# Optimization experiments

Hardware: AMD Instinct MI355X
Metric: run time of the kernel (lower is better)

The kernel has to match this reference:

```python
import jax, jax.numpy as jnp
import numpy as np

N_HEADS = 8
PROJ_DIM = 32


def _phi(x):
    # elu(x) + 1 feature map (always > 0)
    return jax.nn.elu(x) + 1.0


def _causal_linear(pq, pk, v):
    # Faithful to torch _linear_kernelized_attention masked branch:
    #   dpq_l = pq_l - pq_{l-1} (with pq_{-1}=0)
    #   result_l = cumsum_{m<=l} (dpq_m . v_m) * pk_m
    # The torch code materializes (N,H,L,D,D); here the identical math is
    # computed via a per-position scalar c_m = dpq_m . v_m, O(L*D) memory.
    dpq = pq - jnp.concatenate([jnp.zeros_like(pq[..., :1, :]), pq[..., :-1, :]], axis=-2)
    c = jnp.einsum('nhld,nhld->nhl', dpq, v)[..., None]  # (N,H,L,1)
    return jnp.cumsum(c * pk, axis=-2)  # (N,H,L,D)


def _bidir_linear(pq, pk, v):
    # Non-masked linear path: (pk^T v) first, then pq @ (.)
    right = jnp.einsum('nhld,nhle->nhde', pk, v)
    return jnp.einsum('nhqd,nhde->nhqe', pq, right)


def _attention(Y, X, Wq, Wk, Wv, mask):
    N, Lq, Dm = Y.shape
    Lk = X.shape[1]
    H, Pd = N_HEADS, PROJ_DIM
    # torch Linear: x @ W^T
    q = (Y @ Wq.T).reshape(N, Lq, H, Pd).transpose(0, 2, 1, 3)  # (N,H,Lq,Pd)
    k = (X @ Wk.T).reshape(N, Lk, H, Pd).transpose(0, 2, 1, 3)
    v = (X @ Wv.T).reshape(N, Lk, H, Pd).transpose(0, 2, 1, 3)
    pq, pk = _phi(q), _phi(k)
    fn = _causal_linear if mask else _bidir_linear
    num = fn(pq, pk, v)
    den = fn(pq, pk, jnp.ones_like(v))  # v_scale = ones expanded to D
    A = num / den
    return A.transpose(0, 2, 1, 3).reshape(N, Lq, H * Pd)


def setup_inputs() -> dict:
    key = jax.random.key(0)
    kY, kX, kq, kk, kv = jax.random.split(key, 5)
    N, L, dim = 2, 8192, N_HEADS * PROJ_DIM
    scale_in = 0.05            # keep phi(q),phi(k) ~ 1 so denominator stays positive
    scale_w = 1.0 / np.sqrt(dim)
    Y = scale_in * jax.random.normal(kY, (N, L, dim), dtype=jnp.float32)
    X = scale_in * jax.random.normal(kX, (N, L, dim), dtype=jnp.float32)
    Wq = scale_w * jax.random.normal(kq, (dim, dim), dtype=jnp.float32)
    Wk = scale_w * jax.random.normal(kk, (dim, dim), dtype=jnp.float32)
    Wv = scale_w * jax.random.normal(kv, (dim, dim), dtype=jnp.float32)
    return {"Y": Y, "X": X, "Wq": Wq, "Wk": Wk, "Wv": Wv, "mask": 1}


def reference(Y, X, Wq, Wk, Wv, mask):
    return _attention(Y, X, Wq, Wk, Wv, mask)
```

## Files before the change

kernel.cpp:

```cpp
#include <hip/hip_runtime.h>
#include <hip/hip_bf16.h>


typedef __attribute__((ext_vector_type(8))) short short8;
typedef __attribute__((ext_vector_type(4))) float f32x4;

__device__ __forceinline__ float phi_f(float x) {
    return x > 0.f ? x + 1.f : __expf(x);
}
__device__ __forceinline__ unsigned short f2bf(float x) {
    __hip_bfloat16 h = __float2bfloat16(x);
    return *reinterpret_cast<unsigned short*>(&h);
}
__device__ __forceinline__ float bf2f(unsigned short u) {
    return __uint_as_float(((unsigned int)u) << 16);
}

__global__ __launch_bounds__(256) void k_prepw(
        const float* __restrict__ Wq, const float* __restrict__ Wk,
        const float* __restrict__ Wv, unsigned short* __restrict__ Wf)
{
    const int g = blockIdx.x * 256 + threadIdx.x;
    const int mat = g >> 13, cc = g & 8191;
    const float* src = (mat == 0) ? Wq : (mat == 1 ? Wv : Wk);
    const int ln = cc & 15, qd = (cc >> 4) & 3, kt = (cc >> 6) & 7, jt = cc >> 9;
    const float* s = src + (size_t)(jt * 16 + ln) * 256 + kt * 32 + qd * 8;
    f32x4 f0 = __builtin_nontemporal_load((const f32x4*)s);
    f32x4 f1 = __builtin_nontemporal_load((const f32x4*)(s + 4));
    short8 o;
    o[0] = f2bf(f0[0]); o[1] = f2bf(f0[1]); o[2] = f2bf(f0[2]); o[3] = f2bf(f0[3]);
    o[4] = f2bf(f1[0]); o[5] = f2bf(f1[1]); o[6] = f2bf(f1[2]); o[7] = f2bf(f1[3]);
    *(short8*)(Wf + (size_t)g * 8) = o;
}

#define LDA 280

__global__ __launch_bounds__(512, 2) void k_gemm(
        const float* __restrict__ Y, const float* __restrict__ X,
        const unsigned short* __restrict__ Wf,
        unsigned short* __restrict__ pk_out,
        float* __restrict__ c_out, float* __restrict__ cd_out,
        float* __restrict__ tot)
{
    __shared__ __align__(16) unsigned short Ys[65 * LDA];
    __shared__ __align__(16) unsigned short Xs[64 * LDA];
    __shared__ float scc[64][8], scd[64][8];
    __shared__ __align__(16) unsigned short spk[64 * 264];

    const int rb = blockIdx.x;
    const int n = rb >> 7, tpair = rb & 127;
    const int mbase = rb * 64;
    const int tile0 = tpair * 2, lseg0 = tpair * 64;
    const bool hasprev = (tpair != 0);
    const int t = threadIdx.x, w = t >> 6, lane = t & 63;
    const int ln = lane & 15, qd = lane >> 4;

#pragma unroll
    for (int it = 0; it < 16; ++it) {
        const int idx = t + it * 512;
        const int half = idx >> 12, row = (idx >> 6) & 63, c4 = idx & 63;
        const float* s = (half ? X : Y) + (size_t)(mbase + row) * 256 + c4 * 4;
        f32x4 f = __builtin_nontemporal_load((const f32x4*)s);
        ushort4 h4;
        h4.x = f2bf(f[0]); h4.y = f2bf(f[1]); h4.z = f2bf(f[2]); h4.w = f2bf(f[3]);
        unsigned short* dst = half ? Xs : Ys;
        *(ushort4*)&dst[row * LDA + c4 * 4] = h4;
    }
    if (t < 64) {
        const int prow = hasprev ? mbase - 1 : mbase;
        f32x4 f = __builtin_nontemporal_load((const f32x4*)(Y + (size_t)prow * 256 + t * 4));
        ushort4 h4;
        h4.x = f2bf(f[0]); h4.y = f2bf(f[1]); h4.z = f2bf(f[2]); h4.w = f2bf(f[3]);
        *(ushort4*)&Ys[64 * LDA + t * 4] = h4;
    }
    __syncthreads();

    f32x4 aq[2][2][2], av[2][2][2], akk[2][2][2], aqp[2];
#pragma unroll
    for (int t2 = 0; t2 < 2; ++t2)
#pragma unroll
        for (int i = 0; i < 2; ++i)
#pragma unroll
            for (int j = 0; j < 2; ++j) {
                aq[t2][i][j]  = (f32x4){0.f, 0.f, 0.f, 0.f};
                av[t2][i][j]  = (f32x4){0.f, 0.f, 0.f, 0.f};
                akk[t2][i][j] = (f32x4){0.f, 0.f, 0.f, 0.f};
            }
    aqp[0] = (f32x4){0.f, 0.f, 0.f, 0.f};
    aqp[1] = (f32x4){0.f, 0.f, 0.f, 0.f};
    const short8 z8 = {0, 0, 0, 0, 0, 0, 0, 0};
    const short8* W8 = (const short8*)Wf;
    const int jt0 = 2 * w;

    short8 Bq[3][2], Bv[3][2], Bk[3][2];
#define LOADB(slot, kt_)                                                   \
    {                                                                      \
        _Pragma("unroll")                                                  \
        for (int jj = 0; jj < 2; ++jj) {                                   \
            const int jt = jt0 + jj;                                       \
            Bq[slot][jj] = W8[(((0 * 16 + jt) * 8 + (kt_)) << 6) + lane];  \
            Bv[slot][jj] = W8[(((1 * 16 + jt) * 8 + (kt_)) << 6) + lane];  \
            Bk[slot][jj] = W8[(((2 * 16 + jt) * 8 + (kt_)) << 6) + lane];  \
        }                                                                  \
    }
    LOADB(0, 0);
    LOADB(1, 1);

#pragma unroll
    for (int kt = 0; kt < 8; ++kt) {
        if (kt + 2 < 8) LOADB((kt + 2) % 3, kt + 2);
        const int ko = kt * 32 + qd * 8;
        short8 ay[2][2], ax[2][2];
#pragma unroll
        for (int t2 = 0; t2 < 2; ++t2)
#pragma unroll
            for (int i = 0; i < 2; ++i) {
                ay[t2][i] = *(const short8*)&Ys[(t2 * 32 + i * 16 + ln) * LDA + ko];
                ax[t2][i] = *(const short8*)&Xs[(t2 * 32 + i * 16 + ln) * LDA + ko];
            }
        short8 ext = *(const short8*)&Ys[64 * LDA + ko];
        short8 ayp = (ln == 15) ? ext : z8;
        const int sl = kt % 3;
#pragma unroll
        for (int jj = 0; jj < 2; ++jj) {
            aq[0][0][jj] = __builtin_amdgcn_mfma_f32_16x16x32_bf16(ay[0][0], Bq[sl][jj], aq[0][0][jj], 0, 0, 0);
            aq[0][1][jj] = __builtin_amdgcn_mfma_f32_16x16x32_bf16(ay[0][1], Bq[sl][jj], aq[0][1][jj], 0, 0, 0);
            aq[1][0][jj] = __builtin_amdgcn_mfma_f32_16x16x32_bf16(ay[1][0], Bq[sl][jj], aq[1][0][jj], 0, 0, 0);
            aq[1][1][jj] = __builtin_amdgcn_mfma_f32_16x16x32_bf16(ay[1][1], Bq[sl][jj], aq[1][1][jj], 0, 0, 0);
            aqp[jj]      = __builtin_amdgcn_mfma_f32_16x16x32_bf16(ayp,      Bq[sl][jj], aqp[jj],      0, 0, 0);
            av[0][0][jj] = __builtin_amdgcn_mfma_f32_16x16x32_bf16(ax[0][0], Bv[sl][jj], av[0][0][jj], 0, 0, 0);
            av[0][1][jj] = __builtin_amdgcn_mfma_f32_16x16x32_bf16(ax[0][1], Bv[sl][jj], av[0][1][jj], 0, 0, 0);
            av[1][0][jj] = __builtin_amdgcn_mfma_f32_16x16x32_bf16(ax[1][0], Bv[sl][jj], av[1][0][jj], 0, 0, 0);
            av[1][1][jj] = __builtin_amdgcn_mfma_f32_16x16x32_bf16(ax[1][1], Bv[sl][jj], av[1][1][jj], 0, 0, 0);
            akk[0][0][jj] = __builtin_amdgcn_mfma_f32_16x16x32_bf16(ax[0][0], Bk[sl][jj], akk[0][0][jj], 0, 0, 0);
            akk[0][1][jj] = __builtin_amdgcn_mfma_f32_16x16x32_bf16(ax[0][1], Bk[sl][jj], akk[0][1][jj], 0, 0, 0);
            akk[1][0][jj] = __builtin_amdgcn_mfma_f32_16x16x32_bf16(ax[1][0], Bk[sl][jj], akk[1][0][jj], 0, 0, 0);
            akk[1][1][jj] = __builtin_amdgcn_mfma_f32_16x16x32_bf16(ax[1][1], Bk[sl][jj], akk[1][1][jj], 0, 0, 0);
        }
    }
#undef LOADB

#pragma unroll
    for (int t2 = 0; t2 < 2; ++t2)
#pragma unroll
        for (int i = 0; i < 2; ++i)
#pragma unroll
            for (int jj = 0; jj < 2; ++jj)
#pragma unroll
                for (int r = 0; r < 4; ++r) aq[t2][i][jj][r] = phi_f(aq[t2][i][jj][r]);
    float pprev[2];
#pragma unroll
    for (int jj = 0; jj < 2; ++jj) {
        float p15 = __shfl(aqp[jj][3], 48 + ln);
        pprev[jj] = hasprev ? phi_f(p15) : 0.f;
    }

    float cc_[2][2][4], cd_[2][2][4];
#pragma unroll
    for (int t2 = 0; t2 < 2; ++t2)
#pragma unroll
        for (int i = 0; i < 2; ++i)
#pragma unroll
            for (int r = 0; r < 4; ++r) { cc_[t2][i][r] = 0.f; cd_[t2][i][r] = 0.f; }
#pragma unroll
    for (int jj = 0; jj < 2; ++jj) {
        float carry = pprev[jj];
#pragma unroll
        for (int t2 = 0; t2 < 2; ++t2)
#pragma unroll
            for (int i = 0; i < 2; ++i) {
                const float p0 = aq[t2][i][jj][0], p1 = aq[t2][i][jj][1];
                const float p2 = aq[t2][i][jj][2], p3 = aq[t2][i][jj][3];
                const float up3 = __shfl_up(p3, 16);
                const float prev0 = (qd == 0) ? carry : up3;
                const float d0 = p0 - prev0, d1 = p1 - p0, d2 = p2 - p1, d3 = p3 - p2;
                cc_[t2][i][0] += d0 * av[t2][i][jj][0]; cd_[t2][i][0] += d0;
                cc_[t2][i][1] += d1 * av[t2][i][jj][1]; cd_[t2][i][1] += d1;
                cc_[t2][i][2] += d2 * av[t2][i][jj][2]; cd_[t2][i][2] += d2;
                cc_[t2][i][3] += d3 * av[t2][i][jj][3]; cd_[t2][i][3] += d3;
                carry = __shfl(p3, ln + 48);
            }
    }
#pragma unroll
    for (int t2 = 0; t2 < 2; ++t2)
#pragma unroll
        for (int i = 0; i < 2; ++i)
#pragma unroll
            for (int r = 0; r < 4; ++r) {
                float x = cc_[t2][i][r];
                x += __shfl_xor(x, 1); x += __shfl_xor(x, 2);
                x += __shfl_xor(x, 4); x += __shfl_xor(x, 8);
                float y = cd_[t2][i][r];
                y += __shfl_xor(y, 1); y += __shfl_xor(y, 2);
                y += __shfl_xor(y, 4); y += __shfl_xor(y, 8);
                if (ln == 0) {
                    scc[t2 * 32 + i * 16 + qd * 4 + r][w] = x;
                    scd[t2 * 32 + i * 16 + qd * 4 + r][w] = y;
                }
            }
    __syncthreads();
    {
        const int row = t & 63, h = t >> 6;
        const size_t gi = (size_t)(n * 8 + h) * 8192 + lseg0 + row;
        c_out[gi]  = scc[row][h];
        cd_out[gi] = scd[row][h];
    }

#pragma unroll
    for (int t2 = 0; t2 < 2; ++t2)
#pragma unroll
        for (int i = 0; i < 2; ++i)
#pragma unroll
            for (int jj = 0; jj < 2; ++jj)
#pragma unroll
                for (int r = 0; r < 4; ++r) akk[t2][i][jj][r] = phi_f(akk[t2][i][jj][r]);
#pragma unroll
    for (int t2 = 0; t2 < 2; ++t2)
#pragma unroll
        for (int jj = 0; jj < 2; ++jj) {
            float tn = 0.f, td = 0.f;
#pragma unroll
            for (int i = 0; i < 2; ++i)
#pragma unroll
                for (int r = 0; r < 4; ++r) {
                    const int row = t2 * 32 + i * 16 + qd * 4 + r;
                    const float pv = akk[t2][i][jj][r];
                    tn += scc[row][w] * pv;
                    td += scd[row][w] * pv;
                }
            tn += __shfl_xor(tn, 16); tn += __shfl_xor(tn, 32);
            td += __shfl_xor(td, 16); td += __shfl_xor(td, 32);
            if (qd == 0) {
                const int d = jj * 16 + ln;
                const size_t bi = ((size_t)(n * 8 + w) * 256 + tile0 + t2) * 64;
                tot[bi + d]      = tn;
                tot[bi + 32 + d] = td;
            }
        }

#pragma unroll
    for (int t2 = 0; t2 < 2; ++t2)
#pragma unroll
        for (int i = 0; i < 2; ++i)
#pragma unroll
            for (int jj = 0; jj < 2; ++jj)
#pragma unroll
                for (int r = 0; r < 4; ++r)
                    spk[(t2 * 32 + i * 16 + qd * 4 + r) * 264 + w * 32 + jj * 16 + ln]
                        = f2bf(akk[t2][i][jj][r]);
    __syncthreads();
#pragma unroll
    for (int it = 0; it < 4; ++it) {
        const int idx = t + 512 * it;
        const int row = idx >> 5, cg = idx & 31;
        short8 vals = *(const short8*)&spk[row * 264 + cg * 8];
        const int head = cg >> 2, d8 = (cg & 3) * 8;
        *(short8*)(pk_out + ((size_t)(n * 8 + head) * 8192 + lseg0 + row) * 32 + d8) = vals;
    }
}

__global__ __launch_bounds__(256) void k_scan(
        const unsigned short* __restrict__ pk, const float* __restrict__ c,
        const float* __restrict__ cd, const float* __restrict__ tot,
        float* __restrict__ out)
{
    __shared__ __align__(16) unsigned short spk[128 * 32];
    __shared__ float sc[128], sd[128];
    __shared__ float wsum[4][64], stile[4][64];

    const int bx = blockIdx.x, seg = bx >> 6, blk = bx & 63;
    const int n = seg >> 3, h = seg & 7;
    const int t = threadIdx.x, l0 = blk * 128;
    const int wv = t >> 6, lane = t & 63;
    const int T = blk * 4;

    const float* tb = tot + (size_t)seg * 256 * 64 + lane;
    float p0 = 0.f, p1 = 0.f, p2 = 0.f, p3 = 0.f,
          p4 = 0.f, p5 = 0.f, p6 = 0.f, p7 = 0.f;
    int i = wv;
    for (; i + 28 < T; i += 32) {
        p0 += tb[(i)      * 64]; p1 += tb[(i + 4)  * 64];
        p2 += tb[(i + 8)  * 64]; p3 += tb[(i + 12) * 64];
        p4 += tb[(i + 16) * 64]; p5 += tb[(i + 20) * 64];
        p6 += tb[(i + 24) * 64]; p7 += tb[(i + 28) * 64];
    }
    for (; i < T; i += 4) p0 += tb[i * 64];
    wsum[wv][lane]  = ((p0 + p1) + (p2 + p3)) + ((p4 + p5) + (p6 + p7));
    stile[wv][lane] = tb[(T + wv) * 64];

#pragma unroll
    for (int it = 0; it < 2; ++it) {
        const int idx = t + 256 * it;
        *(short8*)&spk[idx * 8] = *(const short8*)(pk + ((size_t)seg * 8192 + l0) * 32 + idx * 8);
    }
    if (t < 128) sc[t] = c[(size_t)seg * 8192 + l0 + t];
    else         sd[t - 128] = cd[(size_t)seg * 8192 + l0 + (t - 128)];
    __syncthreads();

    if (t < 128) {
        const int g = t >> 5, d = t & 31;
        float rn  = (wsum[0][d] + wsum[1][d]) + (wsum[2][d] + wsum[3][d]);
        float rd_ = (wsum[0][32 + d] + wsum[1][32 + d]) + (wsum[2][32 + d] + wsum[3][32 + d]);
#pragma unroll
        for (int i2 = 0; i2 < 3; ++i2)
            if (i2 < g) { rn += stile[i2][d]; rd_ += stile[i2][32 + d]; }
        float* ob = out + ((size_t)n * 8192 + l0 + g * 32) * 256 + h * 32 + d;
#pragma unroll
        for (int p = 0; p < 32; ++p) {
            const int m = g * 32 + p;
            const float pkv = bf2f(spk[m * 32 + d]);
            rn  += sc[m] * pkv;
            rd_ += sd[m] * pkv;
            __builtin_nontemporal_store(rn / rd_, &ob[(size_t)p * 256]);
        }
    }
}

extern "C" void kernel_launch(void* const* d_in, const int* in_sizes, int n_in,
                              void* d_out, int out_size, void* d_ws, size_t ws_size,
                              hipStream_t stream)
{
    const float* Y  = (const float*)d_in[0];
    const float* X  = (const float*)d_in[1];
    const float* Wq = (const float*)d_in[2];
    const float* Wk = (const float*)d_in[3];
    const float* Wv = (const float*)d_in[4];
    float* out = (float*)d_out;

    float* ws = (float*)d_ws;
    unsigned short* Wf = (unsigned short*)ws;
    unsigned short* pk = (unsigned short*)(ws + 98304);
    float* c   = ws + 98304 + 2097152;
    float* cd  = c  + 131072;
    float* tot = cd + 131072;

    hipLaunchKernelGGL(k_prepw, dim3(96),   dim3(256), 0, stream, Wq, Wk, Wv, Wf);
    hipLaunchKernelGGL(k_gemm,  dim3(256),  dim3(512), 0, stream,
                       Y, X, Wf, pk, c, cd, tot);
    hipLaunchKernelGGL(k_scan,  dim3(1024), dim3(256), 0, stream, pk, c, cd, tot, out);
}
```

Measured before the change: 113.7 us.

## Fuse scan into GEMM kernel via cooperative grid sync

Merges the scan kernel into the GEMM kernel using a cooperative launch and a grid-wide barrier. The pk, c and cd intermediates now stay in shared memory instead of going through global memory, and only per-tile totals are exchanged. After the barrier each block computes its own prefix from the totals and writes the output. This removes one kernel launch and the intermediate global traffic, in exchange for a grid sync and a scan phase that runs with fewer threads (256 blocks instead of 1024) while the blocks hold large shared allocations.

```diff
diff --git a/kernel.cpp b/kernel.cpp
--- a/kernel.cpp
+++ b/kernel.cpp
@@ -1,6 +1,9 @@
 #include <hip/hip_runtime.h>
 #include <hip/hip_bf16.h>
-
+#include <hip/hip_cooperative_groups.h>
+
+
+namespace cg = cooperative_groups;
 
 typedef __attribute__((ext_vector_type(8))) short short8;
 typedef __attribute__((ext_vector_type(4))) float f32x4;
@@ -38,9 +41,7 @@
 __global__ __launch_bounds__(512, 2) void k_gemm(
         const float* __restrict__ Y, const float* __restrict__ X,
         const unsigned short* __restrict__ Wf,
-        unsigned short* __restrict__ pk_out,
-        float* __restrict__ c_out, float* __restrict__ cd_out,
-        float* __restrict__ tot)
+        float* __restrict__ tot, float* __restrict__ out)
 {
     __shared__ __align__(16) unsigned short Ys[65 * LDA];
     __shared__ __align__(16) unsigned short Xs[64 * LDA];
@@ -199,12 +200,6 @@
                 }
             }
     __syncthreads();
-    {
-        const int row = t & 63, h = t >> 6;
-        const size_t gi = (size_t)(n * 8 + h) * 8192 + lseg0 + row;
-        c_out[gi]  = scc[row][h];
-        cd_out[gi] = scd[row][h];
-    }
 
 #pragma unroll
     for (int t2 = 0; t2 < 2; ++t2)
@@ -233,8 +228,8 @@
             if (qd == 0) {
                 const int d = jj * 16 + ln;
                 const size_t bi = ((size_t)(n * 8 + w) * 256 + tile0 + t2) * 64;
-                tot[bi + d]      = tn;
-                tot[bi + 32 + d] = td;
+                float2 v; v.x = tn; v.y = td;
+                *(float2*)&tot[bi + 2 * d] = v;
             }
         }
 
@@ -249,69 +244,56 @@
                     spk[(t2 * 32 + i * 16 + qd * 4 + r) * 264 + w * 32 + jj * 16 + ln]
                         = f2bf(akk[t2][i][jj][r]);
     __syncthreads();
-#pragma unroll
-    for (int it = 0; it < 4; ++it) {
-        const int idx = t + 512 * it;
-        const int row = idx >> 5, cg = idx & 31;
-        short8 vals = *(const short8*)&spk[row * 264 + cg * 8];
-        const int head = cg >> 2, d8 = (cg & 3) * 8;
-        *(short8*)(pk_out + ((size_t)(n * 8 + head) * 8192 + lseg0 + row) * 32 + d8) = vals;
-    }
-}
-
-__global__ __launch_bounds__(256) void k_scan(
-        const unsigned short* __restrict__ pk, const float* __restrict__ c,
-        const float* __restrict__ cd, const float* __restrict__ tot,
-        float* __restrict__ out)
-{
-    __shared__ __align__(16) unsigned short spk[128 * 32];
-    __shared__ float sc[128], sd[128];
-    __shared__ float wsum[4][64], stile[4][64];
-
-    const int bx = blockIdx.x, seg = bx >> 6, blk = bx & 63;
-    const int n = seg >> 3, h = seg & 7;
-    const int t = threadIdx.x, l0 = blk * 128;
-    const int wv = t >> 6, lane = t & 63;
-    const int T = blk * 4;
-
-    const float* tb = tot + (size_t)seg * 256 * 64 + lane;
-    float p0 = 0.f, p1 = 0.f, p2 = 0.f, p3 = 0.f,
-          p4 = 0.f, p5 = 0.f, p6 = 0.f, p7 = 0.f;
-    int i = wv;
-    for (; i + 28 < T; i += 32) {
-        p0 += tb[(i)      * 64]; p1 += tb[(i + 4)  * 64];
-        p2 += tb[(i + 8)  * 64]; p3 += tb[(i + 12) * 64];
-        p4 += tb[(i + 16) * 64]; p5 += tb[(i + 20) * 64];
-        p6 += tb[(i + 24) * 64]; p7 += tb[(i + 28) * 64];
-    }
-    for (; i < T; i += 4) p0 += tb[i * 64];
-    wsum[wv][lane]  = ((p0 + p1) + (p2 + p3)) + ((p4 + p5) + (p6 + p7));
-    stile[wv][lane] = tb[(T + wv) * 64];
-
-#pragma unroll
-    for (int it = 0; it < 2; ++it) {
-        const int idx = t + 256 * it;
-        *(short8*)&spk[idx * 8] = *(const short8*)(pk + ((size_t)seg * 8192 + l0) * 32 + idx * 8);
-    }
-    if (t < 128) sc[t] = c[(size_t)seg * 8192 + l0 + t];
-    else         sd[t - 128] = cd[(size_t)seg * 8192 + l0 + (t - 128)];
-    __syncthreads();
-
-    if (t < 128) {
-        const int g = t >> 5, d = t & 31;
-        float rn  = (wsum[0][d] + wsum[1][d]) + (wsum[2][d] + wsum[3][d]);
-        float rd_ = (wsum[0][32 + d] + wsum[1][32 + d]) + (wsum[2][32 + d] + wsum[3][32 + d]);
-#pragma unroll
-        for (int i2 = 0; i2 < 3; ++i2)
-            if (i2 < g) { rn += stile[i2][d]; rd_ += stile[i2][32 + d]; }
-        float* ob = out + ((size_t)n * 8192 + l0 + g * 32) * 256 + h * 32 + d;
+
+    __threadfence();
+    cg::this_grid().sync();
+
+    {
+        const int d = lane & 31, g = lane >> 5;
+        const float* tb = tot + (size_t)(n * 8 + w) * 256 * 64 + 2 * d;
+
+        float sn0 = 0.f, sn1 = 0.f, sn2 = 0.f, sn3 = 0.f;
+        float sn4 = 0.f, sn5 = 0.f, sn6 = 0.f, sn7 = 0.f;
+        float sd0 = 0.f, sd1 = 0.f, sd2 = 0.f, sd3 = 0.f;
+        float sd4 = 0.f, sd5 = 0.f, sd6 = 0.f, sd7 = 0.f;
+        int tt = g * tpair;
+        const int te = tt + tpair;
+        for (; tt + 7 < te; tt += 8) {
+            float2 v0 = *(const float2*)(tb + (size_t)(tt + 0) * 64);
+            float2 v1 = *(const float2*)(tb + (size_t)(tt + 1) * 64);
+            float2 v2 = *(const float2*)(tb + (size_t)(tt + 2) * 64);
+            float2 v3 = *(const float2*)(tb + (size_t)(tt + 3) * 64);
+            float2 v4 = *(const float2*)(tb + (size_t)(tt + 4) * 64);
+            float2 v5 = *(const float2*)(tb + (size_t)(tt + 5) * 64);
+            float2 v6 = *(const float2*)(tb + (size_t)(tt + 6) * 64);
+            float2 v7 = *(const float2*)(tb + (size_t)(tt + 7) * 64);
+            sn0 += v0.x; sd0 += v0.y; sn1 += v1.x; sd1 += v1.y;
+            sn2 += v2.x; sd2 += v2.y; sn3 += v3.x; sd3 += v3.y;
+            sn4 += v4.x; sd4 += v4.y; sn5 += v5.x; sd5 += v5.y;
+            sn6 += v6.x; sd6 += v6.y; sn7 += v7.x; sd7 += v7.y;
+        }
+        for (; tt < te; ++tt) {
+            float2 v = *(const float2*)(tb + (size_t)tt * 64);
+            sn0 += v.x; sd0 += v.y;
+        }
+        float xn = ((sn0 + sn1) + (sn2 + sn3)) + ((sn4 + sn5) + (sn6 + sn7));
+        float xd = ((sd0 + sd1) + (sd2 + sd3)) + ((sd4 + sd5) + (sd6 + sd7));
+        xn += __shfl_xor(xn, 32);
+        xd += __shfl_xor(xd, 32);
+        if (g) {
+            float2 v = *(const float2*)(tb + (size_t)tile0 * 64);
+            xn += v.x; xd += v.y;
+        }
+
+        float rn = xn, rd = xd;
+        float* ob = out + ((size_t)n * 8192 + lseg0 + g * 32) * 256 + w * 32 + d;
 #pragma unroll
         for (int p = 0; p < 32; ++p) {
             const int m = g * 32 + p;
-            const float pkv = bf2f(spk[m * 32 + d]);
-            rn  += sc[m] * pkv;
-            rd_ += sd[m] * pkv;
-            __builtin_nontemporal_store(rn / rd_, &ob[(size_t)p * 256]);
+            const float pkv = bf2f(spk[m * 264 + w * 32 + d]);
+            rn += scc[m][w] * pkv;
+            rd += scd[m][w] * pkv;
+            __builtin_nontemporal_store(rn / rd, &ob[(size_t)p * 256]);
         }
     }
 }
@@ -329,13 +311,11 @@
 
     float* ws = (float*)d_ws;
     unsigned short* Wf = (unsigned short*)ws;
-    unsigned short* pk = (unsigned short*)(ws + 98304);
-    float* c   = ws + 98304 + 2097152;
-    float* cd  = c  + 131072;
-    float* tot = cd + 131072;
-
-    hipLaunchKernelGGL(k_prepw, dim3(96),   dim3(256), 0, stream, Wq, Wk, Wv, Wf);
-    hipLaunchKernelGGL(k_gemm,  dim3(256),  dim3(512), 0, stream,
-                       Y, X, Wf, pk, c, cd, tot);
-    hipLaunchKernelGGL(k_scan,  dim3(1024), dim3(256), 0, stream, pk, c, cd, tot, out);
-}
+    float* tot = ws + 98304;
+
+    hipLaunchKernelGGL(k_prepw, dim3(96), dim3(256), 0, stream, Wq, Wk, Wv, Wf);
+
+    void* args[] = {(void*)&Y, (void*)&X, (void*)&Wf, (void*)&tot, (void*)&out};
+    hipLaunchCooperativeKernel((const void*)k_gemm, dim3(256), dim3(512),
+                               args, 0, stream);
+}
```

Result: slower. 177.5 us (+56.2%).
